# Kernel tuning notes

Hardware: AMD Instinct MI355X
Metric: run time of the kernel (lower is better)

## Reference

```python
import jax, jax.numpy as jnp
import numpy as np

N, E, DIN, DH, HEADS, DOUT = 50000, 800000, 128, 32, 4, 16
NL_HID = 2  # num_layers - 1
HID = HEADS * DH


def setup_inputs() -> dict:
    key = jax.random.key(0)
    ks = jax.random.split(key, 16)

    def w(k, shape, fan_in):
        return jax.random.normal(k, shape, jnp.float32) * (1.0 / np.sqrt(fan_in))

    return {
        "x": jax.random.normal(ks[0], (N, DIN), jnp.float32),
        "edge_index": jax.random.randint(ks[1], (2, E), 0, N, dtype=jnp.int64),
        "edge_attr": jax.random.normal(ks[2], (E, 1), jnp.float32),
        # conv1: dim_in -> (heads, dim_h)
        "W1": w(ks[3], (DIN, HID), DIN),
        "as1": w(ks[4], (HEADS, DH), DH),
        "ad1": w(ks[5], (HEADS, DH), DH),
        "b1": jnp.zeros((HID,), jnp.float32),
        # hidden convs: hid -> (heads, dim_h), stacked over NL_HID layers
        "Wh": w(ks[6], (NL_HID, HID, HID), HID),
        "ash": w(ks[7], (NL_HID, HEADS, DH), DH),
        "adh": w(ks[8], (NL_HID, HEADS, DH), DH),
        "bh": jnp.zeros((NL_HID, HID), jnp.float32),
        # conv2: hid -> (1, dim_out)
        "W2": w(ks[9], (HID, DOUT), HID),
        "as2": w(ks[10], (1, DOUT), DOUT),
        "ad2": w(ks[11], (1, DOUT), DOUT),
        "b2": jnp.zeros((DOUT,), jnp.float32),
    }


def _gat_conv(x, src, dst, W, a_s, a_d, b):
    """PyG GATConv (eval mode: attention dropout inactive), concat heads."""
    H, C = a_s.shape
    n = x.shape[0]
    h = (x @ W).reshape(n, H, C)                       # [N,H,C]
    al_s = jnp.einsum('nhc,hc->nh', h, a_s)            # [N,H]
    al_d = jnp.einsum('nhc,hc->nh', h, a_d)
    e = jax.nn.leaky_relu(al_s[src] + al_d[dst], 0.2)  # [Et,H]
    # scatter-softmax over incoming edges of each destination node
    m = jax.ops.segment_max(e, dst, num_segments=n)
    ee = jnp.exp(e - m[dst])
    denom = jax.ops.segment_sum(ee, dst, num_segments=n)
    alpha = ee / (denom[dst] + 1e-16)                  # [Et,H]
    out = jax.ops.segment_sum(h[src] * alpha[:, :, None], dst, num_segments=n)
    return out.reshape(n, H * C) + b


def reference(x, edge_index, edge_attr, W1, as1, ad1, b1, Wh, ash, adh, bh, W2, as2, ad2, b2):
    n = x.shape[0]
    # GATConv adds self-loops by default
    loops = jnp.arange(n, dtype=edge_index.dtype)
    src = jnp.concatenate([edge_index[0], loops])
    dst = jnp.concatenate([edge_index[1], loops])
    h = jax.nn.elu(_gat_conv(x, src, dst, W1, as1, ad1, b1))
    for i in range(Wh.shape[0]):  # dropout p=0.5 inactive in eval mode
        h = jax.nn.elu(_gat_conv(h, src, dst, Wh[i], ash[i], adh[i], bh[i]))
    return _gat_conv(h, src, dst, W2, as2, ad2, b2)  # heads=1 -> [N, DOUT]
```

## Files before the change

### kernel.cpp

```cpp
#include <hip/hip_runtime.h>
#include <hip/hip_bf16.h>
#include <hip/hip_fp16.h>


typedef _Float16 half8_t __attribute__((ext_vector_type(8)));
typedef float f32x4_t  __attribute__((ext_vector_type(4)));

static inline int divup(int a, int b){ return (a + b - 1) / b; }


__global__ __launch_bounds__(256) void zero_cnt_kernel(int* __restrict__ cnt, int n){
    int i = blockIdx.x * 256 + threadIdx.x;
    int4 z = {0, 0, 0, 0};
    if (i * 4 + 3 < n){
        *(int4*)(cnt + i * 4) = z;
    } else {
        for (int j = i * 4; j < n; ++j) cnt[j] = 0;
    }
}


__global__ __launch_bounds__(256) void fill_sliced_kernel(const int* __restrict__ src,
                                                          const int* __restrict__ dst,
                                                          int* __restrict__ cnt,
                                                          unsigned short* __restrict__ csr,
                                                          int E, int Et){
    int slice = blockIdx.x & 7;
    int e = (blockIdx.x >> 3) * 256 + threadIdx.x;
    if (e >= Et) return;
    int d = (e < E) ? dst[e] : (e - E);
    if (((d >> 4) & 7) != slice) return;
    int s = (e < E) ? src[e] : d;
    int pos = atomicAdd(&cnt[d], 1);
    csr[(d << 6) + pos] = (unsigned short)s;
}


__global__ __launch_bounds__(256) void prep_kernel(const float* __restrict__ W1,
                                                   const float* __restrict__ Wh,
                                                   const float* __restrict__ as1,
                                                   const float* __restrict__ ad1,
                                                   const float* __restrict__ ash,
                                                   const float* __restrict__ adh,
                                                   const float* __restrict__ W2,
                                                   const float* __restrict__ as2,
                                                   const float* __restrict__ ad2,
                                                   _Float16* __restrict__ WTx,
                                                   _Float16* __restrict__ W2x){
    int id = blockIdx.x * 256 + threadIdx.x;
    const int MAIN = 3 * 144 * 128;
    if (id < MAIN){
        int l = id / (144 * 128), rem = id % (144 * 128);
        int c = rem >> 7, k = rem & 127;
        const float* W = (l == 0) ? W1 : (Wh + (size_t)(l - 1) * 16384);
        float v = 0.f;
        if (c < 128){
            v = W[k * 128 + c];
        } else if (c < 136){
            int h = (c - 128) & 3;
            const float* a = (c < 132) ? ((l == 0) ? as1 : ash + (size_t)(l - 1) * 128)
                                       : ((l == 0) ? ad1 : adh + (size_t)(l - 1) * 128);
            const float* wr = W + k * 128 + h * 32;
            const float* ar = a + h * 32;
            float sum = 0.f;
            #pragma unroll
            for (int c2 = 0; c2 < 32; ++c2) sum += wr[c2] * ar[c2];
            v = sum;
        }
        WTx[id] = (_Float16)v;
    } else if (id < MAIN + 32 * 128){
        int id2 = id - MAIN;
        int c = id2 >> 7, k = id2 & 127;
        float v = 0.f;
        if (c < 16){
            v = W2[k * 16 + c];
        } else if (c == 16 || c == 17){
            const float* a = (c == 16) ? as2 : ad2;
            float sum = 0.f;
            #pragma unroll
            for (int j = 0; j < 16; ++j) sum += W2[k * 16 + j] * a[j];
            v = sum;
        }
        W2x[id2] = (_Float16)v;
    }
}


template<bool F32IN>
__device__ __forceinline__ void gemm128L_body(const void* __restrict__ Xv,
                                              const _Float16* __restrict__ WTx,
                                              _Float16* __restrict__ H16,
                                              float* __restrict__ als,
                                              float* __restrict__ ald, int n){
    int wav = threadIdx.x >> 6, lane = threadIdx.x & 63;
    int nb = blockIdx.x * 16;
    int r = lane & 15, kg = lane >> 4;
    int anode = nb + r; if (anode >= n) anode = n - 1;

    half8_t a0, a1, a2, a3;
    if (F32IN){
        const float* xrow = (const float*)Xv + (size_t)anode * 128 + kg * 8;
        #pragma unroll
        for (int q = 0; q < 4; ++q){
            float4 u = *(const float4*)(xrow + q * 32);
            float4 w = *(const float4*)(xrow + q * 32 + 4);
            half8_t o = {(_Float16)u.x,(_Float16)u.y,(_Float16)u.z,(_Float16)u.w,
                         (_Float16)w.x,(_Float16)w.y,(_Float16)w.z,(_Float16)w.w};
            if (q == 0) a0 = o; else if (q == 1) a1 = o; else if (q == 2) a2 = o; else a3 = o;
        }
    } else {
        const _Float16* xrow = (const _Float16*)Xv + (size_t)anode * 128 + kg * 8;
        a0 = *(const half8_t*)(xrow);
        a1 = *(const half8_t*)(xrow + 32);
        a2 = *(const half8_t*)(xrow + 64);
        a3 = *(const half8_t*)(xrow + 96);
    }

    const _Float16* wc0 = WTx + (size_t)(wav * 32 + r) * 128 + kg * 8;
    const _Float16* wc1 = wc0 + 16 * 128;

    f32x4_t c0 = {0.f,0.f,0.f,0.f}, c1 = {0.f,0.f,0.f,0.f};
    c0 = __builtin_amdgcn_mfma_f32_16x16x32_f16(a0, *(const half8_t*)(wc0     ), c0, 0,0,0);
    c1 = __builtin_amdgcn_mfma_f32_16x16x32_f16(a0, *(const half8_t*)(wc1     ), c1, 0,0,0);
    c0 = __builtin_amdgcn_mfma_f32_16x16x32_f16(a1, *(const half8_t*)(wc0 + 32), c0, 0,0,0);
    c1 = __builtin_amdgcn_mfma_f32_16x16x32_f16(a1, *(const half8_t*)(wc1 + 32), c1, 0,0,0);
    c0 = __builtin_amdgcn_mfma_f32_16x16x32_f16(a2, *(const half8_t*)(wc0 + 64), c0, 0,0,0);
    c1 = __builtin_amdgcn_mfma_f32_16x16x32_f16(a2, *(const half8_t*)(wc1 + 64), c1, 0,0,0);
    c0 = __builtin_amdgcn_mfma_f32_16x16x32_f16(a3, *(const half8_t*)(wc0 + 96), c0, 0,0,0);
    c1 = __builtin_amdgcn_mfma_f32_16x16x32_f16(a3, *(const half8_t*)(wc1 + 96), c1, 0,0,0);

    int colw = wav * 32 + r;
    #pragma unroll
    for (int rg = 0; rg < 4; ++rg){
        int onode = nb + kg * 4 + rg;
        if (onode < n){
            _Float16* hr = H16 + (size_t)onode * 128 + colw;
            hr[0]  = (_Float16)c0[rg];
            hr[16] = (_Float16)c1[rg];
        }
    }

    if (wav == 0){
        const _Float16* wl = WTx + (size_t)(128 + r) * 128 + kg * 8;
        f32x4_t cl = {0.f,0.f,0.f,0.f};
        cl = __builtin_amdgcn_mfma_f32_16x16x32_f16(a0, *(const half8_t*)(wl     ), cl, 0,0,0);
        cl = __builtin_amdgcn_mfma_f32_16x16x32_f16(a1, *(const half8_t*)(wl + 32), cl, 0,0,0);
        cl = __builtin_amdgcn_mfma_f32_16x16x32_f16(a2, *(const half8_t*)(wl + 64), cl, 0,0,0);
        cl = __builtin_amdgcn_mfma_f32_16x16x32_f16(a3, *(const half8_t*)(wl + 96), cl, 0,0,0);
        if (r < 8){
            #pragma unroll
            for (int rg = 0; rg < 4; ++rg){
                int onode = nb + kg * 4 + rg;
                if (onode < n){
                    if (r < 4) als[(size_t)onode * 4 + r]       = cl[rg];
                    else       ald[(size_t)onode * 4 + (r - 4)] = cl[rg];
                }
            }
        }
    }
}

__global__ __launch_bounds__(256) void gemm128L_f32_kernel(const float* __restrict__ X,
                                                           const _Float16* __restrict__ WTx,
                                                           _Float16* __restrict__ H16,
                                                           float* __restrict__ als,
                                                           float* __restrict__ ald, int n){
    gemm128L_body<true>(X, WTx, H16, als, ald, n);
}

__global__ __launch_bounds__(256) void gemm128L_f16_kernel(const _Float16* __restrict__ X16,
                                                           const _Float16* __restrict__ WTx,
                                                           _Float16* __restrict__ H16,
                                                           float* __restrict__ als,
                                                           float* __restrict__ ald, int n){
    gemm128L_body<false>(X16, WTx, H16, als, ald, n);
}


__global__ __launch_bounds__(256) void gemm16L_kernel(const _Float16* __restrict__ X16,
                                                      const _Float16* __restrict__ W2x,
                                                      _Float16* __restrict__ H4,
                                                      float* __restrict__ als4,
                                                      float* __restrict__ ald4, int n){
    int wav = threadIdx.x >> 6, lane = threadIdx.x & 63;
    int nb = blockIdx.x * 64 + wav * 16;
    int r = lane & 15, kg = lane >> 4;
    int anode = nb + r; if (anode >= n) anode = n - 1;

    const _Float16* xrow = X16 + (size_t)anode * 128 + kg * 8;
    half8_t a0 = *(const half8_t*)(xrow);
    half8_t a1 = *(const half8_t*)(xrow + 32);
    half8_t a2 = *(const half8_t*)(xrow + 64);
    half8_t a3 = *(const half8_t*)(xrow + 96);

    const _Float16* wc0 = W2x + (size_t)r * 128 + kg * 8;
    const _Float16* wc1 = wc0 + 16 * 128;

    f32x4_t c0 = {0.f,0.f,0.f,0.f}, c1 = {0.f,0.f,0.f,0.f};
    c0 = __builtin_amdgcn_mfma_f32_16x16x32_f16(a0, *(const half8_t*)(wc0     ), c0, 0,0,0);
    c1 = __builtin_amdgcn_mfma_f32_16x16x32_f16(a0, *(const half8_t*)(wc1     ), c1, 0,0,0);
    c0 = __builtin_amdgcn_mfma_f32_16x16x32_f16(a1, *(const half8_t*)(wc0 + 32), c0, 0,0,0);
    c1 = __builtin_amdgcn_mfma_f32_16x16x32_f16(a1, *(const half8_t*)(wc1 + 32), c1, 0,0,0);
    c0 = __builtin_amdgcn_mfma_f32_16x16x32_f16(a2, *(const half8_t*)(wc0 + 64), c0, 0,0,0);
    c1 = __builtin_amdgcn_mfma_f32_16x16x32_f16(a2, *(const half8_t*)(wc1 + 64), c1, 0,0,0);
    c0 = __builtin_amdgcn_mfma_f32_16x16x32_f16(a3, *(const half8_t*)(wc0 + 96), c0, 0,0,0);
    c1 = __builtin_amdgcn_mfma_f32_16x16x32_f16(a3, *(const half8_t*)(wc1 + 96), c1, 0,0,0);

    #pragma unroll
    for (int rg = 0; rg < 4; ++rg){
        int onode = nb + kg * 4 + rg;
        if (onode < n){
            H4[(size_t)onode * 16 + r] = (_Float16)c0[rg];
            if (r == 0) als4[onode] = c1[rg];
            else if (r == 1) ald4[onode] = c1[rg];
        }
    }
}


__global__ __launch_bounds__(256) void aggregate128_kernel(const __half* __restrict__ H16,
                                                           const float* __restrict__ als,
                                                           const float* __restrict__ ald,
                                                           const int* __restrict__ cnt,
                                                           const unsigned short* __restrict__ csr,
                                                           const float* __restrict__ bias,
                                                           _Float16* __restrict__ out16,
                                                           int n){
    int node = blockIdx.x * 4 + (threadIdx.x >> 6);
    int lane = threadIdx.x & 63;
    if (node >= n) return;
    int start = node << 6, end = start + cnt[node];

    int eg = lane >> 4, cl = lane & 15;
    int h = cl >> 2;
    float ad_h = ald[(size_t)node * 4 + h];

    float den = 0.f;
    float acc[8] = {0,0,0,0,0,0,0,0};
    const __half* Hc = H16 + cl * 8;
    int i = start + eg;
    for (; i + 4 < end; i += 8){
        int sA = csr[i];
        int sB = csr[i + 4];
        float eA = als[(size_t)sA * 4 + h] + ad_h; eA = eA > 0.f ? eA : 0.2f * eA;
        float eB = als[(size_t)sB * 4 + h] + ad_h; eB = eB > 0.f ? eB : 0.2f * eB;
        float wA = __expf(eA);
        float wB = __expf(eB);
        den += wA + wB;
        uint4 ra = *(const uint4*)(Hc + (size_t)sA * 128);
        uint4 rb = *(const uint4*)(Hc + (size_t)sB * 128);
        float2 a0 = __half22float2(*(__half2*)&ra.x);
        float2 a1 = __half22float2(*(__half2*)&ra.y);
        float2 a2 = __half22float2(*(__half2*)&ra.z);
        float2 a3 = __half22float2(*(__half2*)&ra.w);
        float2 b0 = __half22float2(*(__half2*)&rb.x);
        float2 b1 = __half22float2(*(__half2*)&rb.y);
        float2 b2 = __half22float2(*(__half2*)&rb.z);
        float2 b3 = __half22float2(*(__half2*)&rb.w);
        acc[0] += wA * a0.x + wB * b0.x; acc[1] += wA * a0.y + wB * b0.y;
        acc[2] += wA * a1.x + wB * b1.x; acc[3] += wA * a1.y + wB * b1.y;
        acc[4] += wA * a2.x + wB * b2.x; acc[5] += wA * a2.y + wB * b2.y;
        acc[6] += wA * a3.x + wB * b3.x; acc[7] += wA * a3.y + wB * b3.y;
    }
    if (i < end){
        int s = csr[i];
        float e = als[(size_t)s * 4 + h] + ad_h; e = e > 0.f ? e : 0.2f * e;
        float w = __expf(e);
        den += w;
        uint4 ra = *(const uint4*)(Hc + (size_t)s * 128);
        float2 a0 = __half22float2(*(__half2*)&ra.x);
        float2 a1 = __half22float2(*(__half2*)&ra.y);
        float2 a2 = __half22float2(*(__half2*)&ra.z);
        float2 a3 = __half22float2(*(__half2*)&ra.w);
        acc[0] += w * a0.x; acc[1] += w * a0.y;
        acc[2] += w * a1.x; acc[3] += w * a1.y;
        acc[4] += w * a2.x; acc[5] += w * a2.y;
        acc[6] += w * a3.x; acc[7] += w * a3.y;
    }
    #pragma unroll
    for (int j = 0; j < 8; ++j){
        acc[j] += __shfl_xor(acc[j], 16);
        acc[j] += __shfl_xor(acc[j], 32);
    }
    den += __shfl_xor(den, 16);
    den += __shfl_xor(den, 32);

    if (eg == 0){
        float inv = 1.f / (den + 1e-16f);
        int col = cl * 8;
        float4 bv0 = *(const float4*)(bias + col);
        float4 bv1 = *(const float4*)(bias + col + 4);
        float v[8];
        v[0] = acc[0]*inv + bv0.x; v[1] = acc[1]*inv + bv0.y;
        v[2] = acc[2]*inv + bv0.z; v[3] = acc[3]*inv + bv0.w;
        v[4] = acc[4]*inv + bv1.x; v[5] = acc[5]*inv + bv1.y;
        v[6] = acc[6]*inv + bv1.z; v[7] = acc[7]*inv + bv1.w;
        #pragma unroll
        for (int j = 0; j < 8; ++j) v[j] = v[j] > 0.f ? v[j] : __expf(v[j]) - 1.f;

        half8_t o16 = {(_Float16)v[0], (_Float16)v[1], (_Float16)v[2], (_Float16)v[3],
                       (_Float16)v[4], (_Float16)v[5], (_Float16)v[6], (_Float16)v[7]};
        *(half8_t*)&out16[(size_t)node * 128 + col] = o16;
    }
}


__global__ __launch_bounds__(256) void aggregate16_kernel(const _Float16* __restrict__ H4,
                                                          const float* __restrict__ als4,
                                                          const float* __restrict__ ald4,
                                                          const int* __restrict__ cnt,
                                                          const unsigned short* __restrict__ csr,
                                                          const float* __restrict__ bias,
                                                          float* __restrict__ out, int n){
    int node = blockIdx.x * 4 + (threadIdx.x >> 6);
    int lane = threadIdx.x & 63;
    if (node >= n) return;
    int start = node << 6, end = start + cnt[node];
    float adn = ald4[node];

    int eg = lane >> 2, cl = lane & 3;
    float den = 0.f;
    float acc0 = 0.f, acc1 = 0.f, acc2 = 0.f, acc3 = 0.f;
    for (int i = start + eg; i < end; i += 16){
        int s = csr[i];
        float e = als4[s] + adn; e = e > 0.f ? e : 0.2f * e;
        float w = __expf(e);
        den += w;
        uint2 hv = *(const uint2*)(H4 + (size_t)s * 16 + cl * 4);
        float2 h0 = __half22float2(*(__half2*)&hv.x);
        float2 h1 = __half22float2(*(__half2*)&hv.y);
        acc0 += w * h0.x; acc1 += w * h0.y; acc2 += w * h1.x; acc3 += w * h1.y;
    }
    #pragma unroll
    for (int off = 4; off <= 32; off <<= 1){
        acc0 += __shfl_xor(acc0, off); acc1 += __shfl_xor(acc1, off);
        acc2 += __shfl_xor(acc2, off); acc3 += __shfl_xor(acc3, off);
        den  += __shfl_xor(den,  off);
    }

    if (eg == 0){
        float inv = 1.f / (den + 1e-16f);
        float4 bv = *(const float4*)(bias + cl * 4);
        float4 o = {acc0*inv + bv.x, acc1*inv + bv.y, acc2*inv + bv.z, acc3*inv + bv.w};
        *(float4*)&out[(size_t)node * 16 + cl * 4] = o;
    }
}


extern "C" void kernel_launch(void* const* d_in, const int* in_sizes, int n_in,
                              void* d_out, int out_size, void* d_ws, size_t ws_size,
                              hipStream_t stream) {
    const float* x   = (const float*)d_in[0];
    const int*   ei  = (const int*)d_in[1];
    const float* W1  = (const float*)d_in[3];
    const float* as1 = (const float*)d_in[4];
    const float* ad1 = (const float*)d_in[5];
    const float* b1  = (const float*)d_in[6];
    const float* Wh  = (const float*)d_in[7];
    const float* ash = (const float*)d_in[8];
    const float* adh = (const float*)d_in[9];
    const float* bh  = (const float*)d_in[10];
    const float* W2  = (const float*)d_in[11];
    const float* as2 = (const float*)d_in[12];
    const float* ad2 = (const float*)d_in[13];
    const float* b2  = (const float*)d_in[14];

    int N = in_sizes[0] / 128;
    int E = in_sizes[1] / 2;
    int Et = E + N;
    const int* srcA = ei;
    const int* dstA = ei + E;

    char* ws = (char*)d_ws;
    size_t off = 0;
    auto alloc = [&](size_t bytes) -> void* {
        void* p = ws + off;
        off = (off + bytes + 255) & ~(size_t)255;
        return p;
    };
    int* cnt      = (int*)alloc((size_t)N * 4);
    unsigned short* csr = (unsigned short*)alloc((size_t)N * 64 * 2);
    _Float16* xbuf16 = (_Float16*)alloc((size_t)N * 128 * 2);
    _Float16* h16    = (_Float16*)alloc((size_t)N * 128 * 2);
    _Float16* wtx    = (_Float16*)alloc((size_t)3 * 144 * 128 * 2);
    _Float16* w2x    = (_Float16*)alloc((size_t)32 * 128 * 2);
    float* als_a  = (float*)alloc((size_t)N * 4 * 4);
    float* ald_a  = (float*)alloc((size_t)N * 4 * 4);
    _Float16* h4  = (_Float16*)alloc((size_t)N * 16 * 2);
    float* als4   = (float*)alloc((size_t)N * 4);
    float* ald4   = (float*)alloc((size_t)N * 4);

    zero_cnt_kernel<<<divup(divup(N, 4), 256), 256, 0, stream>>>(cnt, N);
    prep_kernel<<<divup(3 * 144 * 128 + 32 * 128, 256), 256, 0, stream>>>(
        W1, Wh, as1, ad1, ash, adh, W2, as2, ad2, wtx, w2x);
    fill_sliced_kernel<<<divup(Et, 256) * 8, 256, 0, stream>>>(srcA, dstA, cnt, csr, E, Et);

    float* out = (float*)d_out;
    const size_t WSTRIDE = (size_t)144 * 128;

    gemm128L_f32_kernel<<<divup(N, 16), 256, 0, stream>>>(x, wtx, h16, als_a, ald_a, N);
    aggregate128_kernel<<<divup(N, 4), 256, 0, stream>>>((const __half*)h16, als_a, ald_a, cnt, csr,
                                                        b1, xbuf16, N);
    gemm128L_f16_kernel<<<divup(N, 16), 256, 0, stream>>>(xbuf16, wtx + WSTRIDE, h16, als_a, ald_a, N);
    aggregate128_kernel<<<divup(N, 4), 256, 0, stream>>>((const __half*)h16, als_a, ald_a, cnt, csr,
                                                        bh, xbuf16, N);
    gemm128L_f16_kernel<<<divup(N, 16), 256, 0, stream>>>(xbuf16, wtx + 2 * WSTRIDE, h16, als_a, ald_a, N);
    aggregate128_kernel<<<divup(N, 4), 256, 0, stream>>>((const __half*)h16, als_a, ald_a, cnt, csr,
                                                        bh + 128, xbuf16, N);

    gemm16L_kernel<<<divup(N, 64), 256, 0, stream>>>(xbuf16, w2x, h4, als4, ald4, N);
    aggregate16_kernel<<<divup(N, 4), 256, 0, stream>>>(h4, als4, ald4, cnt, csr, b2, out, N);
}
```

Before: 259.0 us.

## Precompute per-edge attention weights once per node into LDS before aggregation

```diff
diff --git a/kernel.cpp b/kernel.cpp
--- a/kernel.cpp
+++ b/kernel.cpp
@@ -226,27 +226,49 @@
                                                            const float* __restrict__ bias,
                                                            _Float16* __restrict__ out16,
                                                            int n){
-    int node = blockIdx.x * 4 + (threadIdx.x >> 6);
+    __shared__ float wlds[4][64][4];
+    __shared__ int   slds[4][64];
+    int wid = threadIdx.x >> 6;
+    int node = blockIdx.x * 4 + wid;
     int lane = threadIdx.x & 63;
-    if (node >= n) return;
-    int start = node << 6, end = start + cnt[node];
+    bool act = (node < n);
+    int deg = act ? cnt[node] : 0;
+    int start = node << 6;
+
+    int s_lane = 0;
+    float4 w4 = {0.f, 0.f, 0.f, 0.f};
+    if (lane < deg){
+        s_lane = csr[start + lane];
+        float4 a = *(const float4*)(als + (size_t)s_lane * 4);
+        float4 ad4 = *(const float4*)(ald + (size_t)node * 4);
+        float e0 = a.x + ad4.x; e0 = e0 > 0.f ? e0 : 0.2f * e0;
+        float e1 = a.y + ad4.y; e1 = e1 > 0.f ? e1 : 0.2f * e1;
+        float e2 = a.z + ad4.z; e2 = e2 > 0.f ? e2 : 0.2f * e2;
+        float e3 = a.w + ad4.w; e3 = e3 > 0.f ? e3 : 0.2f * e3;
+        w4.x = __expf(e0); w4.y = __expf(e1); w4.z = __expf(e2); w4.w = __expf(e3);
+    }
+    slds[wid][lane] = s_lane;
+    *(float4*)&wlds[wid][lane][0] = w4;
+
+    float d0 = w4.x, d1 = w4.y, d2 = w4.z, d3 = w4.w;
+    #pragma unroll
+    for (int off = 32; off > 0; off >>= 1){
+        d0 += __shfl_xor(d0, off); d1 += __shfl_xor(d1, off);
+        d2 += __shfl_xor(d2, off); d3 += __shfl_xor(d3, off);
+    }
+
+    __syncthreads();
 
     int eg = lane >> 4, cl = lane & 15;
     int h = cl >> 2;
-    float ad_h = ald[(size_t)node * 4 + h];
-
-    float den = 0.f;
     float acc[8] = {0,0,0,0,0,0,0,0};
     const __half* Hc = H16 + cl * 8;
-    int i = start + eg;
-    for (; i + 4 < end; i += 8){
-        int sA = csr[i];
-        int sB = csr[i + 4];
-        float eA = als[(size_t)sA * 4 + h] + ad_h; eA = eA > 0.f ? eA : 0.2f * eA;
-        float eB = als[(size_t)sB * 4 + h] + ad_h; eB = eB > 0.f ? eB : 0.2f * eB;
-        float wA = __expf(eA);
-        float wB = __expf(eB);
-        den += wA + wB;
+    int i = eg;
+    for (; i + 4 < deg; i += 8){
+        int sA = slds[wid][i];
+        int sB = slds[wid][i + 4];
+        float wA = wlds[wid][i][h];
+        float wB = wlds[wid][i + 4][h];
         uint4 ra = *(const uint4*)(Hc + (size_t)sA * 128);
         uint4 rb = *(const uint4*)(Hc + (size_t)sB * 128);
         float2 a0 = __half22float2(*(__half2*)&ra.x);
@@ -262,11 +284,9 @@
         acc[4] += wA * a2.x + wB * b2.x; acc[5] += wA * a2.y + wB * b2.y;
         acc[6] += wA * a3.x + wB * b3.x; acc[7] += wA * a3.y + wB * b3.y;
     }
-    if (i < end){
-        int s = csr[i];
-        float e = als[(size_t)s * 4 + h] + ad_h; e = e > 0.f ? e : 0.2f * e;
-        float w = __expf(e);
-        den += w;
+    if (i < deg){
+        int s = slds[wid][i];
+        float w = wlds[wid][i][h];
         uint4 ra = *(const uint4*)(Hc + (size_t)s * 128);
         float2 a0 = __half22float2(*(__half2*)&ra.x);
         float2 a1 = __half22float2(*(__half2*)&ra.y);
@@ -282,11 +302,10 @@
         acc[j] += __shfl_xor(acc[j], 16);
         acc[j] += __shfl_xor(acc[j], 32);
     }
-    den += __shfl_xor(den, 16);
-    den += __shfl_xor(den, 32);
-
-    if (eg == 0){
-        float inv = 1.f / (den + 1e-16f);
+
+    if (act && eg == 0){
+        float den_h = (h == 0) ? d0 : (h == 1) ? d1 : (h == 2) ? d2 : d3;
+        float inv = 1.f / (den_h + 1e-16f);
         int col = cl * 8;
         float4 bv0 = *(const float4*)(bias + col);
         float4 bv1 = *(const float4*)(bias + col + 4);
@@ -312,20 +331,35 @@
                                                           const unsigned short* __restrict__ csr,
                                                           const float* __restrict__ bias,
                                                           float* __restrict__ out, int n){
-    int node = blockIdx.x * 4 + (threadIdx.x >> 6);
+    __shared__ float w16lds[4][64];
+    __shared__ int   s16lds[4][64];
+    int wid = threadIdx.x >> 6;
+    int node = blockIdx.x * 4 + wid;
     int lane = threadIdx.x & 63;
-    if (node >= n) return;
-    int start = node << 6, end = start + cnt[node];
-    float adn = ald4[node];
+    bool act = (node < n);
+    int deg = act ? cnt[node] : 0;
+    int start = node << 6;
+
+    int s_lane = 0; float w_lane = 0.f;
+    if (lane < deg){
+        s_lane = csr[start + lane];
+        float e = als4[s_lane] + ald4[node]; e = e > 0.f ? e : 0.2f * e;
+        w_lane = __expf(e);
+    }
+    s16lds[wid][lane] = s_lane;
+    w16lds[wid][lane] = w_lane;
+
+    float den = w_lane;
+    #pragma unroll
+    for (int off = 32; off > 0; off >>= 1) den += __shfl_xor(den, off);
+
+    __syncthreads();
 
     int eg = lane >> 2, cl = lane & 3;
-    float den = 0.f;
     float acc0 = 0.f, acc1 = 0.f, acc2 = 0.f, acc3 = 0.f;
-    for (int i = start + eg; i < end; i += 16){
-        int s = csr[i];
-        float e = als4[s] + adn; e = e > 0.f ? e : 0.2f * e;
-        float w = __expf(e);
-        den += w;
+    for (int i = eg; i < deg; i += 16){
+        int s = s16lds[wid][i];
+        float w = w16lds[wid][i];
         uint2 hv = *(const uint2*)(H4 + (size_t)s * 16 + cl * 4);
         float2 h0 = __half22float2(*(__half2*)&hv.x);
         float2 h1 = __half22float2(*(__half2*)&hv.y);
@@ -335,10 +369,9 @@
     for (int off = 4; off <= 32; off <<= 1){
         acc0 += __shfl_xor(acc0, off); acc1 += __shfl_xor(acc1, off);
         acc2 += __shfl_xor(acc2, off); acc3 += __shfl_xor(acc3, off);
-        den  += __shfl_xor(den,  off);
-    }
-
-    if (eg == 0){
+    }
+
+    if (act && eg == 0){
         float inv = 1.f / (den + 1e-16f);
         float4 bv = *(const float4*)(bias + cl * 4);
         float4 o = {acc0*inv + bv.x, acc1*inv + bv.y, acc2*inv + bv.z, acc3*inv + bv.w};
```

After: 266.9 us. 1.03x slower.
